# Performance work log

Measured on AMD Instinct MI355X. Metric: run time of the kernel, lower is better.

Reference implementation:

```python
import jax, jax.numpy as jnp
import numpy as np

T, H, E, I, TOP_K = 4096, 1024, 8, 2048, 2
EPS = 1e-05


def setup_inputs() -> dict:
    key = jax.random.key(0)
    ks = jax.random.split(key, 4)
    x = jax.random.normal(ks[0], (T, H), dtype=jnp.float32)
    scale = jnp.ones((H,), dtype=jnp.float32)
    gate_kernel = jax.random.normal(ks[1], (H, E), dtype=jnp.float32) * (1.0 / np.sqrt(H))
    gate_bias = jnp.zeros((E,), dtype=jnp.float32)
    mlp1_weight = jax.random.normal(ks[2], (E, H, 2 * I), dtype=jnp.float32) * (1.0 / np.sqrt(H))
    mlp1_bias = jnp.zeros((E, 2 * I), dtype=jnp.float32)
    mlp2_weight = jax.random.normal(ks[3], (E, I, H), dtype=jnp.float32) * (1.0 / np.sqrt(I))
    mlp2_bias = jnp.zeros((E, H), dtype=jnp.float32)
    return {"x": x, "scale": scale, "gate_kernel": gate_kernel, "gate_bias": gate_bias,
            "mlp1_weight": mlp1_weight, "mlp1_bias": mlp1_bias,
            "mlp2_weight": mlp2_weight, "mlp2_bias": mlp2_bias}


def _rmsnorm(x, scale):
    t = x.astype(jnp.float32)
    rms = jnp.sqrt(jnp.mean(t * t, axis=-1, keepdims=True) + EPS)
    return ((t / rms) * scale).astype(x.dtype)


def reference(x, scale, gate_kernel, gate_bias, mlp1_weight, mlp1_bias, mlp2_weight, mlp2_bias):
    normed = _rmsnorm(x, scale)                                   # [T, H]
    _ = normed @ gate_kernel + gate_bias                          # gate logits (unused: static routing)
    # dense per-token, all-expert MLP: [T,H] x [E,H,2I] -> [T,E,2I]
    hidden = jnp.einsum('th,ehi->tei', normed, mlp1_weight) + mlp1_bias
    gate = jnp.minimum(hidden[..., :I], 7.0)
    linear = jnp.clip(hidden[..., I:], -7.0, 7.0)
    activated = gate * jax.nn.sigmoid(1.702 * gate) * (linear + 1.0)
    expert_out = jnp.einsum('tei,eih->teh', activated, mlp2_weight) + mlp2_bias  # [T,E,H]
    # static uniform routing over the first TOP_K experts
    mix = jnp.where(jnp.arange(E) < TOP_K, 1.0 / TOP_K, 0.0).astype(x.dtype)     # [E]
    fused = jnp.einsum('teh,e->th', expert_out, mix)
    return x + fused
```

## Files before the change

kernel.cpp:

```cpp
#include <hip/hip_runtime.h>
#include <hip/hip_bf16.h>
#include <stdint.h>

#define T_DIM 4096
#define H_DIM 1024
#define I_DIM 2048

typedef __bf16 bf16x8 __attribute__((ext_vector_type(8)));
typedef float f32x4 __attribute__((ext_vector_type(4)));
typedef unsigned short ushort_t;
typedef unsigned short us4 __attribute__((ext_vector_type(4)));

__device__ __forceinline__ unsigned short f32_to_bf16(float f) {
  unsigned int u = __float_as_uint(f);
  u += 0x7fffu + ((u >> 16) & 1u);
  return (unsigned short)(u >> 16);
}

__device__ __forceinline__ void gload_lds16(const void* g, void* l) {
  __builtin_amdgcn_global_load_lds(
      (__attribute__((address_space(1))) void*)(uintptr_t)g,
      (__attribute__((address_space(3))) void*)(unsigned int)(uintptr_t)l,
      16, 0, 0);
}

#define S_BARRIER() asm volatile("s_barrier" ::: "memory")
#define WAITV(n) asm volatile("s_waitcnt vmcnt(" #n ")" ::: "memory")
#define IRFENCE() asm volatile("" ::: "memory")
#define MFMA16(acc, va, vb) \
  acc = __builtin_amdgcn_mfma_f32_16x16x32_bf16(va, vb, acc, 0, 0, 0)

__global__ __launch_bounds__(256) void k_rmsnorm(const float* __restrict__ x,
                                                 const float* __restrict__ scale,
                                                 ushort_t* __restrict__ normed) {
  const int row = blockIdx.x, tid = threadIdx.x;
  const float4 v = ((const float4*)(x + (size_t)row * H_DIM))[tid];
  float ss = v.x * v.x + v.y * v.y + v.z * v.z + v.w * v.w;
#pragma unroll
  for (int off = 32; off > 0; off >>= 1) ss += __shfl_xor(ss, off);
  __shared__ float wsum[4];
  if ((tid & 63) == 0) wsum[tid >> 6] = ss;
  __syncthreads();
  const float tot = wsum[0] + wsum[1] + wsum[2] + wsum[3];
  const float inv = rsqrtf(tot * (1.0f / H_DIM) + 1e-5f);
  const float4 sc = ((const float4*)scale)[tid];
  us4 o;
  o.x = f32_to_bf16(v.x * inv * sc.x);
  o.y = f32_to_bf16(v.y * inv * sc.y);
  o.z = f32_to_bf16(v.z * inv * sc.z);
  o.w = f32_to_bf16(v.w * inv * sc.w);
  ((us4*)(normed + (size_t)row * H_DIM))[tid] = o;
}

__global__ __launch_bounds__(256) void k_transpose_cvt(const float* __restrict__ src,
                                                       ushort_t* __restrict__ dst,
                                                       int R, int C) {
  __shared__ float tile[32][33];
  const size_t eoff = (size_t)blockIdx.z * (size_t)R * (size_t)C;
  src += eoff;
  dst += eoff;
  const int x0 = blockIdx.x * 32, y0 = blockIdx.y * 32;
  const int tx = threadIdx.x & 31, ty = threadIdx.x >> 5;
#pragma unroll
  for (int i = 0; i < 4; ++i)
    tile[ty + 8 * i][tx] = src[(size_t)(y0 + ty + 8 * i) * C + x0 + tx];
  __syncthreads();
#pragma unroll
  for (int i = 0; i < 4; ++i)
    dst[(size_t)(x0 + ty + 8 * i) * R + y0 + tx] = f32_to_bf16(tile[tx][ty + 8 * i]);
}

__global__ __launch_bounds__(256) void k_init_out(const float* __restrict__ x,
                                                  const float* __restrict__ b2,
                                                  float* __restrict__ out) {
  const int idx = blockIdx.x * 256 + threadIdx.x;
  const int col4 = idx & (H_DIM / 4 - 1);
  const float4 xv = ((const float4*)x)[idx];
  const float4 b0 = ((const float4*)b2)[col4];
  const float4 b1 = ((const float4*)(b2 + H_DIM))[col4];
  float4 o;
  o.x = xv.x + 0.5f * (b0.x + b1.x);
  o.y = xv.y + 0.5f * (b0.y + b1.y);
  o.z = xv.z + 0.5f * (b0.z + b1.z);
  o.w = xv.w + 0.5f * (b0.w + b1.w);
  ((float4*)out)[idx] = o;
}

__global__ __launch_bounds__(512, 2) void k_gemm1_8ph(
    const ushort_t* __restrict__ normed, const ushort_t* __restrict__ w1T,
    const float* __restrict__ b1, ushort_t* __restrict__ act) {
  __shared__ __align__(16) ushort_t lds[2][4][8192];
  const int tid = threadIdx.x;
  const int wg = (blockIdx.x & 7) * 64 + (blockIdx.x >> 3);
  const int e = wg >> 8;
  const int rem = wg & 255;
  const int brow = (rem >> 4) * 256;
  const int bcol = (rem & 15) * 128;
  const int lane = tid & 63;
  const int wm = (tid >> 6) >> 1;
  const int wn = (tid >> 6) & 1;
  const int r16 = lane & 15, kh = lane >> 4;

  const ushort_t* aBase = normed + (size_t)brow * H_DIM;
  const ushort_t* gBase = w1T + ((size_t)e * 2 * I_DIM + bcol) * H_DIM;
  const ushort_t* lBase = gBase + (size_t)I_DIM * H_DIM;

  f32x4 accg[4][4], accl[4][4];
  const f32x4 zf = {0.f, 0.f, 0.f, 0.f};
#pragma unroll
  for (int m = 0; m < 4; ++m)
#pragma unroll
    for (int n = 0; n < 4; ++n) { accg[m][n] = zf; accl[m][n] = zf; }

  auto stageA = [&](int buf, int ksub, int kt) {
#pragma unroll
    for (int j = 0; j < 2; ++j) {
      const int row = j * 128 + (tid >> 2);
      const int col = (tid & 3) * 8;
      gload_lds16(aBase + (size_t)row * H_DIM + kt * 64 + ksub * 32 + col,
                  &lds[buf][ksub * 2][(j * 512 + (tid & ~63)) * 8]);
    }
  };
  auto stageB = [&](int buf, int ksub, int kt) {
    const int row = tid >> 2;
    const int kc = kt * 64 + ksub * 32 + (tid & 3) * 8;
    gload_lds16(gBase + (size_t)row * H_DIM + kc,
                &lds[buf][ksub * 2 + 1][(tid & ~63) * 8]);
    gload_lds16(lBase + (size_t)row * H_DIM + kc,
                &lds[buf][ksub * 2 + 1][4096 + (tid & ~63) * 8]);
  };
  auto rdA = [&](int buf, int ksub, int m) -> bf16x8 {
    const int r = wm * 64 + m * 16 + r16;
    return *(const bf16x8*)&lds[buf][ksub * 2][r * 32 + kh * 8];
  };
  auto rdBg = [&](int buf, int ksub, int n) -> bf16x8 {
    const int r = wn * 64 + n * 16 + r16;
    return *(const bf16x8*)&lds[buf][ksub * 2 + 1][r * 32 + kh * 8];
  };
  auto rdBl = [&](int buf, int ksub, int n) -> bf16x8 {
    const int r = wn * 64 + n * 16 + r16;
    return *(const bf16x8*)&lds[buf][ksub * 2 + 1][4096 + r * 32 + kh * 8];
  };

  stageA(0, 0, 0); IRFENCE();
  stageB(0, 0, 0); IRFENCE();
  stageA(0, 1, 0); IRFENCE();
  stageB(0, 1, 0);
  WAITV(4);
  S_BARRIER();

  bf16x8 a[4], b[4];
#pragma unroll 1
  for (int t = 0; t < 15; ++t) {
    const int cur = t & 1, nxt = cur ^ 1;
#pragma unroll
    for (int m = 0; m < 4; ++m) a[m] = rdA(cur, 0, m);
#pragma unroll
    for (int n = 0; n < 4; ++n) b[n] = rdBg(cur, 0, n);
    stageA(nxt, 0, t + 1);
    S_BARRIER();
    __builtin_amdgcn_s_setprio(1);
#pragma unroll
    for (int m = 0; m < 4; ++m)
#pragma unroll
      for (int n = 0; n < 4; ++n) MFMA16(accg[m][n], a[m], b[n]);
    __builtin_amdgcn_s_setprio(0);
    WAITV(6);
    S_BARRIER();
    __builtin_amdgcn_sched_barrier(0);
#pragma unroll
    for (int n = 0; n < 4; ++n) b[n] = rdBl(cur, 0, n);
    stageB(nxt, 0, t + 1);
    S_BARRIER();
    __builtin_amdgcn_s_setprio(1);
#pragma unroll
    for (int m = 0; m < 4; ++m)
#pragma unroll
      for (int n = 0; n < 4; ++n) MFMA16(accl[m][n], a[m], b[n]);
    __builtin_amdgcn_s_setprio(0);
    WAITV(4);
    S_BARRIER();
    __builtin_amdgcn_sched_barrier(0);
#pragma unroll
    for (int m = 0; m < 4; ++m) a[m] = rdA(cur, 1, m);
#pragma unroll
    for (int n = 0; n < 4; ++n) b[n] = rdBg(cur, 1, n);
    stageA(nxt, 1, t + 1);
    S_BARRIER();
    __builtin_amdgcn_s_setprio(1);
#pragma unroll
    for (int m = 0; m < 4; ++m)
#pragma unroll
      for (int n = 0; n < 4; ++n) MFMA16(accg[m][n], a[m], b[n]);
    __builtin_amdgcn_s_setprio(0);
    WAITV(6);
    S_BARRIER();
    __builtin_amdgcn_sched_barrier(0);
#pragma unroll
    for (int n = 0; n < 4; ++n) b[n] = rdBl(cur, 1, n);
    stageB(nxt, 1, t + 1);
    S_BARRIER();
    __builtin_amdgcn_s_setprio(1);
#pragma unroll
    for (int m = 0; m < 4; ++m)
#pragma unroll
      for (int n = 0; n < 4; ++n) MFMA16(accl[m][n], a[m], b[n]);
    __builtin_amdgcn_s_setprio(0);
    WAITV(4);
    S_BARRIER();
    __builtin_amdgcn_sched_barrier(0);
  }
  {
#pragma unroll
    for (int m = 0; m < 4; ++m) a[m] = rdA(1, 0, m);
#pragma unroll
    for (int n = 0; n < 4; ++n) b[n] = rdBg(1, 0, n);
#pragma unroll
    for (int m = 0; m < 4; ++m)
#pragma unroll
      for (int n = 0; n < 4; ++n) MFMA16(accg[m][n], a[m], b[n]);
#pragma unroll
    for (int n = 0; n < 4; ++n) b[n] = rdBl(1, 0, n);
#pragma unroll
    for (int m = 0; m < 4; ++m)
#pragma unroll
      for (int n = 0; n < 4; ++n) MFMA16(accl[m][n], a[m], b[n]);
    WAITV(0);
    S_BARRIER();
#pragma unroll
    for (int m = 0; m < 4; ++m) a[m] = rdA(1, 1, m);
#pragma unroll
    for (int n = 0; n < 4; ++n) b[n] = rdBg(1, 1, n);
#pragma unroll
    for (int m = 0; m < 4; ++m)
#pragma unroll
      for (int n = 0; n < 4; ++n) MFMA16(accg[m][n], a[m], b[n]);
#pragma unroll
    for (int n = 0; n < 4; ++n) b[n] = rdBl(1, 1, n);
#pragma unroll
    for (int m = 0; m < 4; ++m)
#pragma unroll
      for (int n = 0; n < 4; ++n) MFMA16(accl[m][n], a[m], b[n]);
  }

  const float* b1e = b1 + (size_t)e * 2 * I_DIM;
#pragma unroll
  for (int m = 0; m < 4; ++m)
#pragma unroll
    for (int n = 0; n < 4; ++n) {
      const int gcol = bcol + wn * 64 + n * 16 + r16;
      const float bgb = b1e[gcol];
      const float blb = b1e[I_DIM + gcol];
#pragma unroll
      for (int rr = 0; rr < 4; ++rr) {
        const int grow = brow + wm * 64 + m * 16 + kh * 4 + rr;
        const float hg = accg[m][n][rr] + bgb;
        const float hl = accl[m][n][rr] + blb;
        const float g = fminf(hg, 7.f);
        const float l = fminf(fmaxf(hl, -7.f), 7.f);
        const float s = 1.f / (1.f + __expf(-1.702f * g));
        const float av = g * s * (l + 1.f);
        act[((size_t)e * T_DIM + grow) * I_DIM + gcol] = f32_to_bf16(av);
      }
    }
}

__global__ __launch_bounds__(512, 2) void k_gemm2_8ph(
    const ushort_t* __restrict__ act, const ushort_t* __restrict__ w2T,
    float* __restrict__ out) {
  __shared__ __align__(16) ushort_t lds[2][4][8192];
  const int tid = threadIdx.x;
  const int wg = (blockIdx.x & 7) * 32 + (blockIdx.x >> 3);
  const int kc = wg >> 6;
  const int rem = wg & 63;
  const int brow = (rem >> 2) * 256;
  const int bcol = (rem & 3) * 256;
  const int e = kc >> 1, ih = kc & 1;
  const int lane = tid & 63;
  const int wm = (tid >> 6) >> 2;
  const int wn = (tid >> 6) & 3;
  const int r16 = lane & 15, kh = lane >> 4;

  const ushort_t* aBase = act + ((size_t)e * T_DIM + brow) * I_DIM + ih * 1024;
  const ushort_t* bBase = w2T + ((size_t)e * H_DIM + bcol) * I_DIM + ih * 1024;

  f32x4 acc[8][4];
  const f32x4 zf = {0.f, 0.f, 0.f, 0.f};
#pragma unroll
  for (int m = 0; m < 8; ++m)
#pragma unroll
    for (int n = 0; n < 4; ++n) acc[m][n] = zf;

  auto stageA = [&](int buf, int ksub, int kt) {
#pragma unroll
    for (int j = 0; j < 2; ++j) {
      const int row = j * 128 + (tid >> 2);
      const int col = (tid & 3) * 8;
      gload_lds16(aBase + (size_t)row * I_DIM + kt * 64 + ksub * 32 + col,
                  &lds[buf][ksub * 2][(j * 512 + (tid & ~63)) * 8]);
    }
  };
  auto stageB = [&](int buf, int ksub, int kt) {
#pragma unroll
    for (int j = 0; j < 2; ++j) {
      const int row = j * 128 + (tid >> 2);
      const int col = (tid & 3) * 8;
      gload_lds16(bBase + (size_t)row * I_DIM + kt * 64 + ksub * 32 + col,
                  &lds[buf][ksub * 2 + 1][(j * 512 + (tid & ~63)) * 8]);
    }
  };
  auto rdA = [&](int buf, int ksub, int m) -> bf16x8 {
    const int r = wm * 128 + m * 16 + r16;
    return *(const bf16x8*)&lds[buf][ksub * 2][r * 32 + kh * 8];
  };
  auto rdB = [&](int buf, int ksub, int n) -> bf16x8 {
    const int r = wn * 64 + n * 16 + r16;
    return *(const bf16x8*)&lds[buf][ksub * 2 + 1][r * 32 + kh * 8];
  };

  stageA(0, 0, 0); IRFENCE();
  stageB(0, 0, 0); IRFENCE();
  stageA(0, 1, 0); IRFENCE();
  stageB(0, 1, 0);
  WAITV(4);
  S_BARRIER();

  bf16x8 a[4], b[4];
#pragma unroll 1
  for (int t = 0; t < 15; ++t) {
    const int cur = t & 1, nxt = cur ^ 1;
#pragma unroll
    for (int m = 0; m < 4; ++m) a[m] = rdA(cur, 0, m);
#pragma unroll
    for (int n = 0; n < 4; ++n) b[n] = rdB(cur, 0, n);
    stageA(nxt, 0, t + 1);
    S_BARRIER();
    __builtin_amdgcn_s_setprio(1);
#pragma unroll
    for (int m = 0; m < 4; ++m)
#pragma unroll
      for (int n = 0; n < 4; ++n) MFMA16(acc[m][n], a[m], b[n]);
    __builtin_amdgcn_s_setprio(0);
    WAITV(6);
    S_BARRIER();
    __builtin_amdgcn_sched_barrier(0);
#pragma unroll
    for (int m = 0; m < 4; ++m) a[m] = rdA(cur, 0, m + 4);
    stageB(nxt, 0, t + 1);
    S_BARRIER();
    __builtin_amdgcn_s_setprio(1);
#pragma unroll
    for (int m = 0; m < 4; ++m)
#pragma unroll
      for (int n = 0; n < 4; ++n) MFMA16(acc[m + 4][n], a[m], b[n]);
    __builtin_amdgcn_s_setprio(0);
    WAITV(4);
    S_BARRIER();
    __builtin_amdgcn_sched_barrier(0);
#pragma unroll
    for (int m = 0; m < 4; ++m) a[m] = rdA(cur, 1, m);
#pragma unroll
    for (int n = 0; n < 4; ++n) b[n] = rdB(cur, 1, n);
    stageA(nxt, 1, t + 1);
    S_BARRIER();
    __builtin_amdgcn_s_setprio(1);
#pragma unroll
    for (int m = 0; m < 4; ++m)
#pragma unroll
      for (int n = 0; n < 4; ++n) MFMA16(acc[m][n], a[m], b[n]);
    __builtin_amdgcn_s_setprio(0);
    WAITV(6);
    S_BARRIER();
    __builtin_amdgcn_sched_barrier(0);
#pragma unroll
    for (int m = 0; m < 4; ++m) a[m] = rdA(cur, 1, m + 4);
    stageB(nxt, 1, t + 1);
    S_BARRIER();
    __builtin_amdgcn_s_setprio(1);
#pragma unroll
    for (int m = 0; m < 4; ++m)
#pragma unroll
      for (int n = 0; n < 4; ++n) MFMA16(acc[m + 4][n], a[m], b[n]);
    __builtin_amdgcn_s_setprio(0);
    WAITV(4);
    S_BARRIER();
    __builtin_amdgcn_sched_barrier(0);
  }
  {
#pragma unroll
    for (int m = 0; m < 4; ++m) a[m] = rdA(1, 0, m);
#pragma unroll
    for (int n = 0; n < 4; ++n) b[n] = rdB(1, 0, n);
#pragma unroll
    for (int m = 0; m < 4; ++m)
#pragma unroll
      for (int n = 0; n < 4; ++n) MFMA16(acc[m][n], a[m], b[n]);
#pragma unroll
    for (int m = 0; m < 4; ++m) a[m] = rdA(1, 0, m + 4);
#pragma unroll
    for (int m = 0; m < 4; ++m)
#pragma unroll
      for (int n = 0; n < 4; ++n) MFMA16(acc[m + 4][n], a[m], b[n]);
    WAITV(0);
    S_BARRIER();
#pragma unroll
    for (int m = 0; m < 4; ++m) a[m] = rdA(1, 1, m);
#pragma unroll
    for (int n = 0; n < 4; ++n) b[n] = rdB(1, 1, n);
#pragma unroll
    for (int m = 0; m < 4; ++m)
#pragma unroll
      for (int n = 0; n < 4; ++n) MFMA16(acc[m][n], a[m], b[n]);
#pragma unroll
    for (int m = 0; m < 4; ++m) a[m] = rdA(1, 1, m + 4);
#pragma unroll
    for (int m = 0; m < 4; ++m)
#pragma unroll
      for (int n = 0; n < 4; ++n) MFMA16(acc[m + 4][n], a[m], b[n]);
  }

#pragma unroll
  for (int m = 0; m < 8; ++m)
#pragma unroll
    for (int n = 0; n < 4; ++n) {
      const int gcol = bcol + wn * 64 + n * 16 + r16;
#pragma unroll
      for (int rr = 0; rr < 4; ++rr) {
        const int grow = brow + wm * 128 + m * 16 + kh * 4 + rr;
        atomicAdd(&out[(size_t)grow * H_DIM + gcol], 0.5f * acc[m][n][rr]);
      }
    }
}

extern "C" void kernel_launch(void* const* d_in, const int* in_sizes, int n_in,
                              void* d_out, int out_size, void* d_ws, size_t ws_size,
                              hipStream_t stream) {
  const float* x = (const float*)d_in[0];
  const float* scale = (const float*)d_in[1];
  const float* w1 = (const float*)d_in[4];
  const float* b1 = (const float*)d_in[5];
  const float* w2 = (const float*)d_in[6];
  const float* b2 = (const float*)d_in[7];
  float* out = (float*)d_out;

  ushort_t* ws = (ushort_t*)d_ws;
  ushort_t* normed = ws;
  ushort_t* w1T = normed + (size_t)T_DIM * H_DIM;
  ushort_t* w2T = w1T + (size_t)2 * 2 * I_DIM * H_DIM;
  ushort_t* actb = w2T + (size_t)2 * H_DIM * I_DIM;

  k_rmsnorm<<<dim3(T_DIM), 256, 0, stream>>>(x, scale, normed);
  k_transpose_cvt<<<dim3(2 * I_DIM / 32, H_DIM / 32, 2), 256, 0, stream>>>(
      w1, w1T, H_DIM, 2 * I_DIM);
  k_transpose_cvt<<<dim3(H_DIM / 32, I_DIM / 32, 2), 256, 0, stream>>>(
      w2, w2T, I_DIM, H_DIM);
  k_init_out<<<dim3(T_DIM * H_DIM / 4 / 256), 256, 0, stream>>>(x, b2, out);
  k_gemm1_8ph<<<dim3(512), 512, 0, stream>>>(normed, w1T, b1, actb);
  k_gemm2_8ph<<<dim3(256), 512, 0, stream>>>(actb, w2T, out);
}
```

Before: 178.4 us.

## Swizzle LDS tiles to avoid bank conflicts and retile gemm2 without K-split

```diff
diff --git a/kernel.cpp b/kernel.cpp
--- a/kernel.cpp
+++ b/kernel.cpp
@@ -23,6 +23,8 @@
       (__attribute__((address_space(3))) void*)(unsigned int)(uintptr_t)l,
       16, 0, 0);
 }
+
+__device__ __forceinline__ int swz(int L) { return L ^ (((L >> 7) & 7) << 4); }
 
 #define S_BARRIER() asm volatile("s_barrier" ::: "memory")
 #define WAITV(n) asm volatile("s_waitcnt vmcnt(" #n ")" ::: "memory")
@@ -112,34 +114,46 @@
 #pragma unroll
     for (int n = 0; n < 4; ++n) { accg[m][n] = zf; accl[m][n] = zf; }
 
+  int srow[2], scolb[2];
+#pragma unroll
+  for (int j = 0; j < 2; ++j) {
+    const int u = swz((j * 512 + tid) * 16);
+    srow[j] = u >> 6;
+    scolb[j] = (u & 63) >> 1;
+  }
+  const int ldst0 = (tid & ~63) * 16;
+
   auto stageA = [&](int buf, int ksub, int kt) {
-#pragma unroll
-    for (int j = 0; j < 2; ++j) {
-      const int row = j * 128 + (tid >> 2);
-      const int col = (tid & 3) * 8;
-      gload_lds16(aBase + (size_t)row * H_DIM + kt * 64 + ksub * 32 + col,
-                  &lds[buf][ksub * 2][(j * 512 + (tid & ~63)) * 8]);
-    }
+    const int kc = kt * 64 + ksub * 32;
+#pragma unroll
+    for (int j = 0; j < 2; ++j)
+      gload_lds16(aBase + (size_t)srow[j] * H_DIM + kc + scolb[j],
+                  (char*)&lds[buf][ksub * 2][0] + j * 8192 + ldst0);
   };
   auto stageB = [&](int buf, int ksub, int kt) {
-    const int row = tid >> 2;
-    const int kc = kt * 64 + ksub * 32 + (tid & 3) * 8;
-    gload_lds16(gBase + (size_t)row * H_DIM + kc,
-                &lds[buf][ksub * 2 + 1][(tid & ~63) * 8]);
-    gload_lds16(lBase + (size_t)row * H_DIM + kc,
-                &lds[buf][ksub * 2 + 1][4096 + (tid & ~63) * 8]);
-  };
+    const int kc = kt * 64 + ksub * 32;
+    gload_lds16(gBase + (size_t)srow[0] * H_DIM + kc + scolb[0],
+                (char*)&lds[buf][ksub * 2 + 1][0] + ldst0);
+    gload_lds16(lBase + (size_t)(srow[1] - 128) * H_DIM + kc + scolb[1],
+                (char*)&lds[buf][ksub * 2 + 1][0] + 8192 + ldst0);
+  };
+
+  int aoffs[4], boffs[4];
+#pragma unroll
+  for (int m = 0; m < 4; ++m)
+    aoffs[m] = swz((wm * 64 + m * 16 + r16) * 64 + kh * 16);
+#pragma unroll
+  for (int n = 0; n < 4; ++n)
+    boffs[n] = swz((wn * 64 + n * 16 + r16) * 64 + kh * 16);
+
   auto rdA = [&](int buf, int ksub, int m) -> bf16x8 {
-    const int r = wm * 64 + m * 16 + r16;
-    return *(const bf16x8*)&lds[buf][ksub * 2][r * 32 + kh * 8];
+    return *(const bf16x8*)((const char*)&lds[buf][ksub * 2][0] + aoffs[m]);
   };
   auto rdBg = [&](int buf, int ksub, int n) -> bf16x8 {
-    const int r = wn * 64 + n * 16 + r16;
-    return *(const bf16x8*)&lds[buf][ksub * 2 + 1][r * 32 + kh * 8];
+    return *(const bf16x8*)((const char*)&lds[buf][ksub * 2 + 1][0] + boffs[n]);
   };
   auto rdBl = [&](int buf, int ksub, int n) -> bf16x8 {
-    const int r = wn * 64 + n * 16 + r16;
-    return *(const bf16x8*)&lds[buf][ksub * 2 + 1][4096 + r * 32 + kh * 8];
+    return *(const bf16x8*)((const char*)&lds[buf][ksub * 2 + 1][0] + 8192 + boffs[n]);
   };
 
   stageA(0, 0, 0); IRFENCE();
@@ -268,72 +282,82 @@
 __global__ __launch_bounds__(512, 2) void k_gemm2_8ph(
     const ushort_t* __restrict__ act, const ushort_t* __restrict__ w2T,
     float* __restrict__ out) {
-  __shared__ __align__(16) ushort_t lds[2][4][8192];
+  __shared__ __align__(16) ushort_t lds[2][2][12288];
   const int tid = threadIdx.x;
   const int wg = (blockIdx.x & 7) * 32 + (blockIdx.x >> 3);
-  const int kc = wg >> 6;
-  const int rem = wg & 63;
-  const int brow = (rem >> 2) * 256;
-  const int bcol = (rem & 3) * 256;
-  const int e = kc >> 1, ih = kc & 1;
+  const int e = wg >> 7;
+  const int tileid = wg & 127;
+  const int brow = (tileid >> 3) * 256;
+  const int bcol = (tileid & 7) * 128;
   const int lane = tid & 63;
-  const int wm = (tid >> 6) >> 2;
-  const int wn = (tid >> 6) & 3;
+  const int wm = (tid >> 6) >> 1;
+  const int wn = (tid >> 6) & 1;
   const int r16 = lane & 15, kh = lane >> 4;
 
-  const ushort_t* aBase = act + ((size_t)e * T_DIM + brow) * I_DIM + ih * 1024;
-  const ushort_t* bBase = w2T + ((size_t)e * H_DIM + bcol) * I_DIM + ih * 1024;
-
-  f32x4 acc[8][4];
+  const ushort_t* aBase = act + ((size_t)e * T_DIM + brow) * I_DIM;
+  const ushort_t* bBase = w2T + ((size_t)e * H_DIM + bcol) * I_DIM;
+
+  f32x4 acc[4][4];
   const f32x4 zf = {0.f, 0.f, 0.f, 0.f};
 #pragma unroll
-  for (int m = 0; m < 8; ++m)
+  for (int m = 0; m < 4; ++m)
 #pragma unroll
     for (int n = 0; n < 4; ++n) acc[m][n] = zf;
 
+  int srow[2], scolb[2];
+#pragma unroll
+  for (int j = 0; j < 2; ++j) {
+    const int u = swz((j * 512 + tid) * 16);
+    srow[j] = u >> 6;
+    scolb[j] = (u & 63) >> 1;
+  }
+  const int ldst0 = (tid & ~63) * 16;
+
   auto stageA = [&](int buf, int ksub, int kt) {
-#pragma unroll
-    for (int j = 0; j < 2; ++j) {
-      const int row = j * 128 + (tid >> 2);
-      const int col = (tid & 3) * 8;
-      gload_lds16(aBase + (size_t)row * I_DIM + kt * 64 + ksub * 32 + col,
-                  &lds[buf][ksub * 2][(j * 512 + (tid & ~63)) * 8]);
-    }
+    const int kc = kt * 64 + ksub * 32;
+#pragma unroll
+    for (int j = 0; j < 2; ++j)
+      gload_lds16(aBase + (size_t)srow[j] * I_DIM + kc + scolb[j],
+                  (char*)&lds[buf][ksub][0] + j * 8192 + ldst0);
   };
   auto stageB = [&](int buf, int ksub, int kt) {
-#pragma unroll
-    for (int j = 0; j < 2; ++j) {
-      const int row = j * 128 + (tid >> 2);
-      const int col = (tid & 3) * 8;
-      gload_lds16(bBase + (size_t)row * I_DIM + kt * 64 + ksub * 32 + col,
-                  &lds[buf][ksub * 2 + 1][(j * 512 + (tid & ~63)) * 8]);
-    }
-  };
+    const int kc = kt * 64 + ksub * 32;
+    gload_lds16(bBase + (size_t)srow[0] * I_DIM + kc + scolb[0],
+                (char*)&lds[buf][ksub][0] + 16384 + ldst0);
+  };
+
+  int aoffs[4], boffs[4];
+#pragma unroll
+  for (int m = 0; m < 4; ++m)
+    aoffs[m] = swz((wm * 64 + m * 16 + r16) * 64 + kh * 16);
+#pragma unroll
+  for (int n = 0; n < 4; ++n)
+    boffs[n] = swz((wn * 64 + n * 16 + r16) * 64 + kh * 16);
+
   auto rdA = [&](int buf, int ksub, int m) -> bf16x8 {
-    const int r = wm * 128 + m * 16 + r16;
-    return *(const bf16x8*)&lds[buf][ksub * 2][r * 32 + kh * 8];
+    return *(const bf16x8*)((const char*)&lds[buf][ksub][0] + aoffs[m]);
   };
   auto rdB = [&](int buf, int ksub, int n) -> bf16x8 {
-    const int r = wn * 64 + n * 16 + r16;
-    return *(const bf16x8*)&lds[buf][ksub * 2 + 1][r * 32 + kh * 8];
+    return *(const bf16x8*)((const char*)&lds[buf][ksub][0] + 16384 + boffs[n]);
   };
 
   stageA(0, 0, 0); IRFENCE();
   stageB(0, 0, 0); IRFENCE();
   stageA(0, 1, 0); IRFENCE();
   stageB(0, 1, 0);
-  WAITV(4);
+  WAITV(3);
   S_BARRIER();
 
   bf16x8 a[4], b[4];
 #pragma unroll 1
-  for (int t = 0; t < 15; ++t) {
+  for (int t = 0; t < 31; ++t) {
     const int cur = t & 1, nxt = cur ^ 1;
 #pragma unroll
     for (int m = 0; m < 4; ++m) a[m] = rdA(cur, 0, m);
 #pragma unroll
     for (int n = 0; n < 4; ++n) b[n] = rdB(cur, 0, n);
     stageA(nxt, 0, t + 1);
+    stageB(nxt, 0, t + 1);
     S_BARRIER();
     __builtin_amdgcn_s_setprio(1);
 #pragma unroll
@@ -341,20 +365,7 @@
 #pragma unroll
       for (int n = 0; n < 4; ++n) MFMA16(acc[m][n], a[m], b[n]);
     __builtin_amdgcn_s_setprio(0);
-    WAITV(6);
-    S_BARRIER();
-    __builtin_amdgcn_sched_barrier(0);
-#pragma unroll
-    for (int m = 0; m < 4; ++m) a[m] = rdA(cur, 0, m + 4);
-    stageB(nxt, 0, t + 1);
-    S_BARRIER();
-    __builtin_amdgcn_s_setprio(1);
-#pragma unroll
-    for (int m = 0; m < 4; ++m)
-#pragma unroll
-      for (int n = 0; n < 4; ++n) MFMA16(acc[m + 4][n], a[m], b[n]);
-    __builtin_amdgcn_s_setprio(0);
-    WAITV(4);
+    WAITV(3);
     S_BARRIER();
     __builtin_amdgcn_sched_barrier(0);
 #pragma unroll
@@ -362,6 +373,7 @@
 #pragma unroll
     for (int n = 0; n < 4; ++n) b[n] = rdB(cur, 1, n);
     stageA(nxt, 1, t + 1);
+    stageB(nxt, 1, t + 1);
     S_BARRIER();
     __builtin_amdgcn_s_setprio(1);
 #pragma unroll
@@ -369,20 +381,7 @@
 #pragma unroll
       for (int n = 0; n < 4; ++n) MFMA16(acc[m][n], a[m], b[n]);
     __builtin_amdgcn_s_setprio(0);
-    WAITV(6);
-    S_BARRIER();
-    __builtin_amdgcn_sched_barrier(0);
-#pragma unroll
-    for (int m = 0; m < 4; ++m) a[m] = rdA(cur, 1, m + 4);
-    stageB(nxt, 1, t + 1);
-    S_BARRIER();
-    __builtin_amdgcn_s_setprio(1);
-#pragma unroll
-    for (int m = 0; m < 4; ++m)
-#pragma unroll
-      for (int n = 0; n < 4; ++n) MFMA16(acc[m + 4][n], a[m], b[n]);
-    __builtin_amdgcn_s_setprio(0);
-    WAITV(4);
+    WAITV(3);
     S_BARRIER();
     __builtin_amdgcn_sched_barrier(0);
   }
@@ -395,12 +394,6 @@
     for (int m = 0; m < 4; ++m)
 #pragma unroll
       for (int n = 0; n < 4; ++n) MFMA16(acc[m][n], a[m], b[n]);
-#pragma unroll
-    for (int m = 0; m < 4; ++m) a[m] = rdA(1, 0, m + 4);
-#pragma unroll
-    for (int m = 0; m < 4; ++m)
-#pragma unroll
-      for (int n = 0; n < 4; ++n) MFMA16(acc[m + 4][n], a[m], b[n]);
     WAITV(0);
     S_BARRIER();
 #pragma unroll
@@ -411,22 +404,16 @@
     for (int m = 0; m < 4; ++m)
 #pragma unroll
       for (int n = 0; n < 4; ++n) MFMA16(acc[m][n], a[m], b[n]);
-#pragma unroll
-    for (int m = 0; m < 4; ++m) a[m] = rdA(1, 1, m + 4);
-#pragma unroll
-    for (int m = 0; m < 4; ++m)
-#pragma unroll
-      for (int n = 0; n < 4; ++n) MFMA16(acc[m + 4][n], a[m], b[n]);
-  }
-
-#pragma unroll
-  for (int m = 0; m < 8; ++m)
+  }
+
+#pragma unroll
+  for (int m = 0; m < 4; ++m)
 #pragma unroll
     for (int n = 0; n < 4; ++n) {
       const int gcol = bcol + wn * 64 + n * 16 + r16;
 #pragma unroll
       for (int rr = 0; rr < 4; ++rr) {
-        const int grow = brow + wm * 128 + m * 16 + kh * 4 + rr;
+        const int grow = brow + wm * 64 + m * 16 + kh * 4 + rr;
         atomicAdd(&out[(size_t)grow * H_DIM + gcol], 0.5f * acc[m][n][rr]);
       }
     }
```

Result: faster. 155.6 us (-12.8%).
